# Kernel tuning notes

Measured on AMD Instinct MI355X. Metric: run time of the kernel, lower is better.

The kernel has to match this reference:

```python
import jax, jax.numpy as jnp
import numpy as np

# SNNConfig constants (see init_kwargs)
TAU_MEM = 0.02
TAU_SYN = 0.005
DT = 0.001
THRESHOLD = 1.0
BETA = 10.0  # fast-sigmoid surrogate beta

BATCH, TIME, IN_DIM, HIDDEN = 32, 1024, 512, 512


@jax.custom_vjp
def spike_fn(v):
    """Heaviside spike with fast-sigmoid surrogate gradient."""
    return (v > THRESHOLD).astype(v.dtype)


def _spike_fwd(v):
    return spike_fn(v), v


def _spike_bwd(v, g):
    x = v - THRESHOLD
    surr = 1.0 / jnp.square(1.0 + BETA * jnp.abs(x))
    return (g * surr,)


spike_fn.defvjp(_spike_fwd, _spike_bwd)


def setup_inputs() -> dict:
    key = jax.random.key(0)
    k1, k2 = jax.random.split(key)
    spikes = jax.random.uniform(k1, (BATCH, TIME, IN_DIM), dtype=jnp.float32)
    # xavier_uniform for (IN_DIM, HIDDEN)
    limit = np.sqrt(6.0 / (IN_DIM + HIDDEN))
    W = jax.random.uniform(k2, (IN_DIM, HIDDEN), dtype=jnp.float32,
                           minval=-limit, maxval=limit)
    b = jnp.zeros((HIDDEN,), dtype=jnp.float32)
    return {"spikes": spikes, "W": W, "b": b}


def reference(spikes, W, b):
    # spikes: [B, T, I]; W: [I, H]; b: [H]
    alpha_mem = jnp.exp(jnp.asarray(-DT / TAU_MEM, dtype=spikes.dtype))
    alpha_syn = jnp.exp(jnp.asarray(-DT / TAU_SYN, dtype=spikes.dtype))
    # hoist the per-step GEMM into one big contraction: [B, T, H]
    I_in = jnp.einsum('bti,ih->bth', spikes, W) + b

    B, T, H = I_in.shape
    v0 = jnp.zeros((B, H), dtype=spikes.dtype)
    s0 = jnp.zeros((B, H), dtype=spikes.dtype)

    def lif_step(carry, i_t):
        v_mem, i_syn = carry
        i_syn = alpha_syn * i_syn + i_t
        v_mem = alpha_mem * v_mem + i_syn
        out = spike_fn(v_mem)
        v_mem = v_mem - out * THRESHOLD  # soft reset
        return (v_mem, i_syn), out

    _, out_spikes = jax.lax.scan(lif_step, (v0, s0), I_in.transpose(1, 0, 2))
    return out_spikes.transpose(1, 0, 2)  # [B, T, H]
```

## Files before the change

### kernel.cpp

```cpp
#include <hip/hip_runtime.h>
#include <hip/hip_bf16.h>

constexpr int BATCH  = 32;
constexpr int TIME   = 1024;
constexpr int IN_DIM = 512;
constexpr int HIDDEN = 512;

constexpr int GM = BATCH * TIME;
constexpr int GN = HIDDEN;
constexpr int GK = IN_DIM;

constexpr int BM = 128;
constexpr int BN = 128;
constexpr int BK = 16;
constexpr int LDAs = BM + 4;
constexpr int LDBs = BN + 4;

__global__ __launch_bounds__(256) void sgemm_bias_kernel(
    const float* __restrict__ A,
    const float* __restrict__ B,
    const float* __restrict__ bias,
    float* __restrict__ C)
{
    __shared__ __align__(16) float As[BK * LDAs];
    __shared__ __align__(16) float Bs[BK * LDBs];

    const int tid = threadIdx.x;
    const int bm  = blockIdx.y * BM;
    const int bn  = blockIdx.x * BN;

    const int w    = tid >> 6;
    const int lane = tid & 63;
    const int row0 = (w >> 1) * 64 + (lane >> 3) * 8;
    const int col0 = (w & 1)  * 64 + (lane & 7)  * 8;

    float acc[8][8];
    #pragma unroll
    for (int i = 0; i < 8; ++i)
        #pragma unroll
        for (int j = 0; j < 8; ++j) acc[i][j] = 0.0f;

    for (int k0 = 0; k0 < GK; k0 += BK) {
        float4 va[2], vb[2];
        #pragma unroll
        for (int i = 0; i < 2; ++i) {
            const int q  = tid + i * 256;
            const int ar = q >> 2;
            const int ac = (q & 3) << 2;
            va[i] = *reinterpret_cast<const float4*>(
                A + (size_t)(bm + ar) * GK + k0 + ac);
            const int br = q >> 5;
            const int bc = (q & 31) << 2;
            vb[i] = *reinterpret_cast<const float4*>(
                B + (size_t)(k0 + br) * GN + bn + bc);
        }

        __syncthreads();

        #pragma unroll
        for (int i = 0; i < 2; ++i) {
            const int q  = tid + i * 256;
            const int ar = q >> 2;
            const int ac = (q & 3) << 2;
            As[(ac + 0) * LDAs + ar] = va[i].x;
            As[(ac + 1) * LDAs + ar] = va[i].y;
            As[(ac + 2) * LDAs + ar] = va[i].z;
            As[(ac + 3) * LDAs + ar] = va[i].w;
            const int br = q >> 5;
            const int bc = (q & 31) << 2;
            *reinterpret_cast<float4*>(&Bs[br * LDBs + bc]) = vb[i];
        }

        __syncthreads();

        #pragma unroll
        for (int kk = 0; kk < BK; ++kk) {
            const float4 a0 = *reinterpret_cast<const float4*>(&As[kk * LDAs + row0]);
            const float4 a1 = *reinterpret_cast<const float4*>(&As[kk * LDAs + row0 + 4]);
            const float4 b0 = *reinterpret_cast<const float4*>(&Bs[kk * LDBs + col0]);
            const float4 b1 = *reinterpret_cast<const float4*>(&Bs[kk * LDBs + col0 + 4]);
            const float ar[8] = {a0.x, a0.y, a0.z, a0.w, a1.x, a1.y, a1.z, a1.w};
            const float br[8] = {b0.x, b0.y, b0.z, b0.w, b1.x, b1.y, b1.z, b1.w};
            #pragma unroll
            for (int i = 0; i < 8; ++i)
                #pragma unroll
                for (int j = 0; j < 8; ++j)
                    acc[i][j] = fmaf(ar[i], br[j], acc[i][j]);
        }
    }

    #pragma unroll
    for (int i = 0; i < 8; ++i) {
        const size_t r = (size_t)(bm + row0 + i);
        #pragma unroll
        for (int j = 0; j < 8; j += 4) {
            float4 v;
            v.x = __fadd_rn(acc[i][j + 0], bias[bn + col0 + j + 0]);
            v.y = __fadd_rn(acc[i][j + 1], bias[bn + col0 + j + 1]);
            v.z = __fadd_rn(acc[i][j + 2], bias[bn + col0 + j + 2]);
            v.w = __fadd_rn(acc[i][j + 3], bias[bn + col0 + j + 3]);
            *reinterpret_cast<float4*>(&C[r * GN + bn + col0 + j]) = v;
        }
    }
}

__global__ __launch_bounds__(64) void lif_scan_kernel(
    const float* __restrict__ I,
    float* __restrict__ O)
{
    const int idx = blockIdx.x * 64 + threadIdx.x;
    const int b = idx >> 9;
    const int h = idx & 511;

    const size_t base = (size_t)b * TIME * HIDDEN + h;
    const float* Ip = I + base;
    float*       Op = O + base;

    const float am = 0.95122942450071400910f;
    const float as = 0.81873075307798185867f;

    float v = 0.0f, s = 0.0f;

    #pragma unroll 1
    for (int t = 0; t < TIME; t += 16) {
        float buf[16];
        #pragma unroll
        for (int u = 0; u < 16; ++u)
            buf[u] = Ip[(size_t)(t + u) * HIDDEN];

        float ob[16];
        #pragma unroll
        for (int u = 0; u < 16; ++u) {
            s = __fadd_rn(__fmul_rn(as, s), buf[u]);
            v = __fadd_rn(__fmul_rn(am, v), s);
            const float o = (v > 1.0f) ? 1.0f : 0.0f;
            v = __fsub_rn(v, o);
            ob[u] = o;
        }

        #pragma unroll
        for (int u = 0; u < 16; ++u)
            Op[(size_t)(t + u) * HIDDEN] = ob[u];
    }
}

extern "C" void kernel_launch(void* const* d_in, const int* in_sizes, int n_in,
                              void* d_out, int out_size, void* d_ws, size_t ws_size,
                              hipStream_t stream) {
    const float* spikes = (const float*)d_in[0];
    const float* W      = (const float*)d_in[1];
    const float* bias   = (const float*)d_in[2];
    float* out  = (float*)d_out;
    float* I_in = (float*)d_ws;

    dim3 g1(GN / BN, GM / BM);
    sgemm_bias_kernel<<<g1, 256, 0, stream>>>(spikes, W, bias, I_in);

    lif_scan_kernel<<<BATCH * HIDDEN / 64, 64, 0, stream>>>(I_in, out);
}
```

Before: 340.9 us.

## Double-buffer GEMM shared tiles and prefetch LIF scan input chunks

The SGEMM now keeps two shared-memory buffers and loads the next K tile into registers while computing on the current one, which removes one barrier per iteration. It also swaps the grid mapping so blockIdx.x walks M, and requests 4 blocks per SIMD via launch bounds. The LIF scan kernel prefetches 32-step input chunks into a second register buffer while the current chunk is processed, so more global loads are in flight. Register pressure rises on both kernels, which could cause spilling under the launch bound or lower occupancy.

```diff
diff --git a/kernel.cpp b/kernel.cpp
--- a/kernel.cpp
+++ b/kernel.cpp
@@ -16,23 +16,37 @@
 constexpr int LDAs = BM + 4;
 constexpr int LDBs = BN + 4;
 
-__global__ __launch_bounds__(256) void sgemm_bias_kernel(
+__global__ __launch_bounds__(256, 4) void sgemm_bias_kernel(
     const float* __restrict__ A,
     const float* __restrict__ B,
     const float* __restrict__ bias,
     float* __restrict__ C)
 {
-    __shared__ __align__(16) float As[BK * LDAs];
-    __shared__ __align__(16) float Bs[BK * LDBs];
+    __shared__ __align__(16) float As[2][BK * LDAs];
+    __shared__ __align__(16) float Bs[2][BK * LDBs];
 
     const int tid = threadIdx.x;
-    const int bm  = blockIdx.y * BM;
-    const int bn  = blockIdx.x * BN;
+    const int bm  = blockIdx.x * BM;
+    const int bn  = blockIdx.y * BN;
 
     const int w    = tid >> 6;
     const int lane = tid & 63;
     const int row0 = (w >> 1) * 64 + (lane >> 3) * 8;
     const int col0 = (w & 1)  * 64 + (lane & 7)  * 8;
+
+    const int ar0 = tid >> 2;
+    const int ac  = (tid & 3) << 2;
+    const int br0 = tid >> 5;
+    const int bc  = (tid & 31) << 2;
+
+    float4 va[2], vb[2];
+
+    auto load_tile = [&](int k0) {
+        va[0] = *reinterpret_cast<const float4*>(A + (size_t)(bm + ar0) * GK + k0 + ac);
+        va[1] = *reinterpret_cast<const float4*>(A + (size_t)(bm + ar0 + 64) * GK + k0 + ac);
+        vb[0] = *reinterpret_cast<const float4*>(B + (size_t)(k0 + br0) * GN + bn + bc);
+        vb[1] = *reinterpret_cast<const float4*>(B + (size_t)(k0 + br0 + 8) * GN + bn + bc);
+    };
 
     float acc[8][8];
     #pragma unroll
@@ -40,52 +54,45 @@
         #pragma unroll
         for (int j = 0; j < 8; ++j) acc[i][j] = 0.0f;
 
-    for (int k0 = 0; k0 < GK; k0 += BK) {
-        float4 va[2], vb[2];
-        #pragma unroll
-        for (int i = 0; i < 2; ++i) {
-            const int q  = tid + i * 256;
-            const int ar = q >> 2;
-            const int ac = (q & 3) << 2;
-            va[i] = *reinterpret_cast<const float4*>(
-                A + (size_t)(bm + ar) * GK + k0 + ac);
-            const int br = q >> 5;
-            const int bc = (q & 31) << 2;
-            vb[i] = *reinterpret_cast<const float4*>(
-                B + (size_t)(k0 + br) * GN + bn + bc);
+    load_tile(0);
+
+    constexpr int NTILES = GK / BK;
+    #pragma unroll 1
+    for (int it = 0; it < NTILES; ++it) {
+        const int p = it & 1;
+        float* asp = As[p];
+        float* bsp = Bs[p];
+
+        {
+            asp[(ac + 0) * LDAs + ar0] = va[0].x;
+            asp[(ac + 1) * LDAs + ar0] = va[0].y;
+            asp[(ac + 2) * LDAs + ar0] = va[0].z;
+            asp[(ac + 3) * LDAs + ar0] = va[0].w;
+            asp[(ac + 0) * LDAs + ar0 + 64] = va[1].x;
+            asp[(ac + 1) * LDAs + ar0 + 64] = va[1].y;
+            asp[(ac + 2) * LDAs + ar0 + 64] = va[1].z;
+            asp[(ac + 3) * LDAs + ar0 + 64] = va[1].w;
+            *reinterpret_cast<float4*>(&bsp[br0 * LDBs + bc]) = vb[0];
+            *reinterpret_cast<float4*>(&bsp[(br0 + 8) * LDBs + bc]) = vb[1];
         }
 
         __syncthreads();
 
-        #pragma unroll
-        for (int i = 0; i < 2; ++i) {
-            const int q  = tid + i * 256;
-            const int ar = q >> 2;
-            const int ac = (q & 3) << 2;
-            As[(ac + 0) * LDAs + ar] = va[i].x;
-            As[(ac + 1) * LDAs + ar] = va[i].y;
-            As[(ac + 2) * LDAs + ar] = va[i].z;
-            As[(ac + 3) * LDAs + ar] = va[i].w;
-            const int br = q >> 5;
-            const int bc = (q & 31) << 2;
-            *reinterpret_cast<float4*>(&Bs[br * LDBs + bc]) = vb[i];
-        }
-
-        __syncthreads();
+        if (it + 1 < NTILES) load_tile((it + 1) * BK);
 
         #pragma unroll
         for (int kk = 0; kk < BK; ++kk) {
-            const float4 a0 = *reinterpret_cast<const float4*>(&As[kk * LDAs + row0]);
-            const float4 a1 = *reinterpret_cast<const float4*>(&As[kk * LDAs + row0 + 4]);
-            const float4 b0 = *reinterpret_cast<const float4*>(&Bs[kk * LDBs + col0]);
-            const float4 b1 = *reinterpret_cast<const float4*>(&Bs[kk * LDBs + col0 + 4]);
-            const float ar[8] = {a0.x, a0.y, a0.z, a0.w, a1.x, a1.y, a1.z, a1.w};
-            const float br[8] = {b0.x, b0.y, b0.z, b0.w, b1.x, b1.y, b1.z, b1.w};
+            const float4 a0 = *reinterpret_cast<const float4*>(&asp[kk * LDAs + row0]);
+            const float4 a1 = *reinterpret_cast<const float4*>(&asp[kk * LDAs + row0 + 4]);
+            const float4 b0 = *reinterpret_cast<const float4*>(&bsp[kk * LDBs + col0]);
+            const float4 b1 = *reinterpret_cast<const float4*>(&bsp[kk * LDBs + col0 + 4]);
+            const float arr[8] = {a0.x, a0.y, a0.z, a0.w, a1.x, a1.y, a1.z, a1.w};
+            const float brr[8] = {b0.x, b0.y, b0.z, b0.w, b1.x, b1.y, b1.z, b1.w};
             #pragma unroll
             for (int i = 0; i < 8; ++i)
                 #pragma unroll
                 for (int j = 0; j < 8; ++j)
-                    acc[i][j] = fmaf(ar[i], br[j], acc[i][j]);
+                    acc[i][j] = fmaf(arr[i], brr[j], acc[i][j]);
         }
     }
 
@@ -104,6 +111,9 @@
     }
 }
 
+constexpr int CH = 32;
+constexpr int NCH = TIME / CH;
+
 __global__ __launch_bounds__(64) void lif_scan_kernel(
     const float* __restrict__ I,
     float* __restrict__ O)
@@ -120,27 +130,53 @@
     const float as = 0.81873075307798185867f;
 
     float v = 0.0f, s = 0.0f;
+    float bufA[CH], bufB[CH];
+
+    #pragma unroll
+    for (int u = 0; u < CH; ++u)
+        bufA[u] = Ip[(size_t)u * HIDDEN];
 
     #pragma unroll 1
-    for (int t = 0; t < TIME; t += 16) {
-        float buf[16];
+    for (int c = 0; c < NCH; c += 2) {
         #pragma unroll
-        for (int u = 0; u < 16; ++u)
-            buf[u] = Ip[(size_t)(t + u) * HIDDEN];
+        for (int u = 0; u < CH; ++u)
+            bufB[u] = Ip[(size_t)((c + 1) * CH + u) * HIDDEN];
 
-        float ob[16];
-        #pragma unroll
-        for (int u = 0; u < 16; ++u) {
-            s = __fadd_rn(__fmul_rn(as, s), buf[u]);
-            v = __fadd_rn(__fmul_rn(am, v), s);
-            const float o = (v > 1.0f) ? 1.0f : 0.0f;
-            v = __fsub_rn(v, o);
-            ob[u] = o;
+        {
+            float ob[CH];
+            #pragma unroll
+            for (int u = 0; u < CH; ++u) {
+                s = __fadd_rn(__fmul_rn(as, s), bufA[u]);
+                v = __fadd_rn(__fmul_rn(am, v), s);
+                const float o = (v > 1.0f) ? 1.0f : 0.0f;
+                v = __fsub_rn(v, o);
+                ob[u] = o;
+            }
+            #pragma unroll
+            for (int u = 0; u < CH; ++u)
+                Op[(size_t)(c * CH + u) * HIDDEN] = ob[u];
         }
 
-        #pragma unroll
-        for (int u = 0; u < 16; ++u)
-            Op[(size_t)(t + u) * HIDDEN] = ob[u];
+        if (c + 2 < NCH) {
+            #pragma unroll
+            for (int u = 0; u < CH; ++u)
+                bufA[u] = Ip[(size_t)((c + 2) * CH + u) * HIDDEN];
+        }
+
+        {
+            float ob[CH];
+            #pragma unroll
+            for (int u = 0; u < CH; ++u) {
+                s = __fadd_rn(__fmul_rn(as, s), bufB[u]);
+                v = __fadd_rn(__fmul_rn(am, v), s);
+                const float o = (v > 1.0f) ? 1.0f : 0.0f;
+                v = __fsub_rn(v, o);
+                ob[u] = o;
+            }
+            #pragma unroll
+            for (int u = 0; u < CH; ++u)
+                Op[(size_t)((c + 1) * CH + u) * HIDDEN] = ob[u];
+        }
     }
 }
 
@@ -153,7 +189,7 @@
     float* out  = (float*)d_out;
     float* I_in = (float*)d_ws;
 
-    dim3 g1(GN / BN, GM / BM);
+    dim3 g1(GM / BM, GN / BN);
     sgemm_bias_kernel<<<g1, 256, 0, stream>>>(spikes, W, bias, I_in);
 
     lif_scan_kernel<<<BATCH * HIDDEN / 64, 64, 0, stream>>>(I_in, out);
```

New measurement: 1.054 ms. 209% more time.

## Fuse GEMM and LIF scan into one warp-specialized kernel with LDS ring

Applied to the files above, without the earlier changes.

Replaces the separate SGEMM and scan kernels with a single kernel. Each block owns one batch and 64 hidden units. Four waves compute 256-timestep chunks of the input current into a double-buffered LDS ring, while a fifth wave runs the LIF recurrence on the previous chunk in lockstep through shared barriers. This removes the 64 MB intermediate write and read-back and the second launch. In exchange it uses about 149 KB of LDS per block, so only one block fits per CU, with only four compute waves and little latency hiding. It also uses a narrower 64-column tile, which makes A be re-read more often.

```diff
diff --git a/kernel.cpp b/kernel.cpp
--- a/kernel.cpp
+++ b/kernel.cpp
@@ -6,141 +6,150 @@
 constexpr int IN_DIM = 512;
 constexpr int HIDDEN = 512;
 
-constexpr int GM = BATCH * TIME;
-constexpr int GN = HIDDEN;
-constexpr int GK = IN_DIM;
+constexpr int TC   = 256;
+constexpr int NC   = TIME / TC;
+constexpr int BK   = 16;
+constexpr int NKT  = IN_DIM / BK;
+constexpr int LDA2 = TC + 4;
+constexpr int LDB2 = 64 + 4;
 
-constexpr int BM = 128;
-constexpr int BN = 128;
-constexpr int BK = 16;
-constexpr int LDAs = BM + 4;
-constexpr int LDBs = BN + 4;
+__global__ __launch_bounds__(320) void fused_lif_kernel(
+    const float* __restrict__ A,
+    const float* __restrict__ Bw,
+    const float* __restrict__ bias,
+    float* __restrict__ O)
+{
+    __shared__ __align__(16) float As[BK * LDA2];
+    __shared__ __align__(16) float Bs[BK * LDB2];
+    __shared__ __align__(16) float ring[2][TC * 64];
 
-__global__ __launch_bounds__(256) void sgemm_bias_kernel(
-    const float* __restrict__ A,
-    const float* __restrict__ B,
-    const float* __restrict__ bias,
-    float* __restrict__ C)
-{
-    __shared__ __align__(16) float As[BK * LDAs];
-    __shared__ __align__(16) float Bs[BK * LDBs];
+    const int blk  = blockIdx.x;
+    const int b    = blk >> 3;
+    const int h0   = (blk & 7) * 64;
+    const int wave = threadIdx.x >> 6;
+    const int lane = threadIdx.x & 63;
 
-    const int tid = threadIdx.x;
-    const int bm  = blockIdx.y * BM;
-    const int bn  = blockIdx.x * BN;
+    const float* Ab = A + (size_t)b * TIME * IN_DIM;
 
-    const int w    = tid >> 6;
-    const int lane = tid & 63;
-    const int row0 = (w >> 1) * 64 + (lane >> 3) * 8;
-    const int col0 = (w & 1)  * 64 + (lane & 7)  * 8;
+    if (wave < 4) {
+        const int tid = threadIdx.x;
+        const int ar = tid >> 2;
+        const int ac = (tid & 3) << 2;
+        const int br = tid >> 4;
+        const int bc = (tid & 15) << 2;
+        const int row0 = wave * 64 + (lane >> 3) * 8;
+        const int col0 = (lane & 7) * 8;
 
-    float acc[8][8];
-    #pragma unroll
-    for (int i = 0; i < 8; ++i)
-        #pragma unroll
-        for (int j = 0; j < 8; ++j) acc[i][j] = 0.0f;
+        float4 va[4], vb;
+        auto load_tile = [&](int c, int kt) {
+            const float* Ap = Ab + (size_t)(c * TC) * IN_DIM + kt * BK;
+            #pragma unroll
+            for (int q = 0; q < 4; ++q)
+                va[q] = *reinterpret_cast<const float4*>(
+                    Ap + (size_t)(ar + 64 * q) * IN_DIM + ac);
+            vb = *reinterpret_cast<const float4*>(
+                Bw + (size_t)(kt * BK + br) * HIDDEN + h0 + bc);
+        };
+        auto store_tile = [&]() {
+            #pragma unroll
+            for (int q = 0; q < 4; ++q) {
+                As[(ac + 0) * LDA2 + ar + 64 * q] = va[q].x;
+                As[(ac + 1) * LDA2 + ar + 64 * q] = va[q].y;
+                As[(ac + 2) * LDA2 + ar + 64 * q] = va[q].z;
+                As[(ac + 3) * LDA2 + ar + 64 * q] = va[q].w;
+            }
+            *reinterpret_cast<float4*>(&Bs[br * LDB2 + bc]) = vb;
+        };
 
-    for (int k0 = 0; k0 < GK; k0 += BK) {
-        float4 va[2], vb[2];
-        #pragma unroll
-        for (int i = 0; i < 2; ++i) {
-            const int q  = tid + i * 256;
-            const int ar = q >> 2;
-            const int ac = (q & 3) << 2;
-            va[i] = *reinterpret_cast<const float4*>(
-                A + (size_t)(bm + ar) * GK + k0 + ac);
-            const int br = q >> 5;
-            const int bc = (q & 31) << 2;
-            vb[i] = *reinterpret_cast<const float4*>(
-                B + (size_t)(k0 + br) * GN + bn + bc);
-        }
-
-        __syncthreads();
-
-        #pragma unroll
-        for (int i = 0; i < 2; ++i) {
-            const int q  = tid + i * 256;
-            const int ar = q >> 2;
-            const int ac = (q & 3) << 2;
-            As[(ac + 0) * LDAs + ar] = va[i].x;
-            As[(ac + 1) * LDAs + ar] = va[i].y;
-            As[(ac + 2) * LDAs + ar] = va[i].z;
-            As[(ac + 3) * LDAs + ar] = va[i].w;
-            const int br = q >> 5;
-            const int bc = (q & 31) << 2;
-            *reinterpret_cast<float4*>(&Bs[br * LDBs + bc]) = vb[i];
-        }
-
-        __syncthreads();
-
-        #pragma unroll
-        for (int kk = 0; kk < BK; ++kk) {
-            const float4 a0 = *reinterpret_cast<const float4*>(&As[kk * LDAs + row0]);
-            const float4 a1 = *reinterpret_cast<const float4*>(&As[kk * LDAs + row0 + 4]);
-            const float4 b0 = *reinterpret_cast<const float4*>(&Bs[kk * LDBs + col0]);
-            const float4 b1 = *reinterpret_cast<const float4*>(&Bs[kk * LDBs + col0 + 4]);
-            const float ar[8] = {a0.x, a0.y, a0.z, a0.w, a1.x, a1.y, a1.z, a1.w};
-            const float br[8] = {b0.x, b0.y, b0.z, b0.w, b1.x, b1.y, b1.z, b1.w};
+        #pragma unroll 1
+        for (int c = 0; c < NC; ++c) {
+            float acc[8][8];
             #pragma unroll
             for (int i = 0; i < 8; ++i)
                 #pragma unroll
-                for (int j = 0; j < 8; ++j)
-                    acc[i][j] = fmaf(ar[i], br[j], acc[i][j]);
+                for (int j = 0; j < 8; ++j) acc[i][j] = 0.0f;
+
+            load_tile(c, 0);
+
+            #pragma unroll 1
+            for (int kt = 0; kt < NKT; ++kt) {
+                __syncthreads();
+                store_tile();
+                if (kt + 1 < NKT) load_tile(c, kt + 1);
+                __syncthreads();
+
+                #pragma unroll
+                for (int kk = 0; kk < BK; ++kk) {
+                    const float4 a0 = *reinterpret_cast<const float4*>(&As[kk * LDA2 + row0]);
+                    const float4 a1 = *reinterpret_cast<const float4*>(&As[kk * LDA2 + row0 + 4]);
+                    const float4 b0 = *reinterpret_cast<const float4*>(&Bs[kk * LDB2 + col0]);
+                    const float4 b1 = *reinterpret_cast<const float4*>(&Bs[kk * LDB2 + col0 + 4]);
+                    const float arr[8] = {a0.x, a0.y, a0.z, a0.w, a1.x, a1.y, a1.z, a1.w};
+                    const float brr[8] = {b0.x, b0.y, b0.z, b0.w, b1.x, b1.y, b1.z, b1.w};
+                    #pragma unroll
+                    for (int i = 0; i < 8; ++i)
+                        #pragma unroll
+                        for (int j = 0; j < 8; ++j)
+                            acc[i][j] = fmaf(arr[i], brr[j], acc[i][j]);
+                }
+            }
+
+            float* rp = ring[c & 1];
+            #pragma unroll
+            for (int i = 0; i < 8; ++i) {
+                #pragma unroll
+                for (int j = 0; j < 8; j += 4) {
+                    float4 v;
+                    v.x = __fadd_rn(acc[i][j + 0], bias[h0 + col0 + j + 0]);
+                    v.y = __fadd_rn(acc[i][j + 1], bias[h0 + col0 + j + 1]);
+                    v.z = __fadd_rn(acc[i][j + 2], bias[h0 + col0 + j + 2]);
+                    v.w = __fadd_rn(acc[i][j + 3], bias[h0 + col0 + j + 3]);
+                    *reinterpret_cast<float4*>(&rp[(row0 + i) * 64 + col0 + j]) = v;
+                }
+            }
+            __syncthreads();
         }
-    }
+    } else {
+        const float am = 0.95122942450071400910f;
+        const float as = 0.81873075307798185867f;
+        float v = 0.0f, s = 0.0f;
+        float* o0 = O + (size_t)b * TIME * HIDDEN + h0 + lane;
 
-    #pragma unroll
-    for (int i = 0; i < 8; ++i) {
-        const size_t r = (size_t)(bm + row0 + i);
-        #pragma unroll
-        for (int j = 0; j < 8; j += 4) {
-            float4 v;
-            v.x = __fadd_rn(acc[i][j + 0], bias[bn + col0 + j + 0]);
-            v.y = __fadd_rn(acc[i][j + 1], bias[bn + col0 + j + 1]);
-            v.z = __fadd_rn(acc[i][j + 2], bias[bn + col0 + j + 2]);
-            v.w = __fadd_rn(acc[i][j + 3], bias[bn + col0 + j + 3]);
-            *reinterpret_cast<float4*>(&C[r * GN + bn + col0 + j]) = v;
+        auto slice = [&](const float* rp, int tbase, int tglob) {
+            float xb[8];
+            #pragma unroll
+            for (int u = 0; u < 8; ++u)
+                xb[u] = rp[(tbase + u) * 64 + lane];
+            float ob[8];
+            #pragma unroll
+            for (int u = 0; u < 8; ++u) {
+                s = __fadd_rn(__fmul_rn(as, s), xb[u]);
+                v = __fadd_rn(__fmul_rn(am, v), s);
+                const float o = (v > 1.0f) ? 1.0f : 0.0f;
+                v = __fsub_rn(v, o);
+                ob[u] = o;
+            }
+            #pragma unroll
+            for (int u = 0; u < 8; ++u)
+                o0[(size_t)(tglob + u) * HIDDEN] = ob[u];
+        };
+
+        #pragma unroll 1
+        for (int c = 0; c < NC; ++c) {
+            const float* rp = ring[(c + 1) & 1];
+            #pragma unroll 1
+            for (int kt = 0; kt < NKT; ++kt) {
+                __syncthreads();
+                __syncthreads();
+                if (c > 0)
+                    slice(rp, kt * 8, (c - 1) * TC + kt * 8);
+            }
+            __syncthreads();
         }
-    }
-}
-
-__global__ __launch_bounds__(64) void lif_scan_kernel(
-    const float* __restrict__ I,
-    float* __restrict__ O)
-{
-    const int idx = blockIdx.x * 64 + threadIdx.x;
-    const int b = idx >> 9;
-    const int h = idx & 511;
-
-    const size_t base = (size_t)b * TIME * HIDDEN + h;
-    const float* Ip = I + base;
-    float*       Op = O + base;
-
-    const float am = 0.95122942450071400910f;
-    const float as = 0.81873075307798185867f;
-
-    float v = 0.0f, s = 0.0f;
-
-    #pragma unroll 1
-    for (int t = 0; t < TIME; t += 16) {
-        float buf[16];
-        #pragma unroll
-        for (int u = 0; u < 16; ++u)
-            buf[u] = Ip[(size_t)(t + u) * HIDDEN];
-
-        float ob[16];
-        #pragma unroll
-        for (int u = 0; u < 16; ++u) {
-            s = __fadd_rn(__fmul_rn(as, s), buf[u]);
-            v = __fadd_rn(__fmul_rn(am, v), s);
-            const float o = (v > 1.0f) ? 1.0f : 0.0f;
-            v = __fsub_rn(v, o);
-            ob[u] = o;
-        }
-
-        #pragma unroll
-        for (int u = 0; u < 16; ++u)
-            Op[(size_t)(t + u) * HIDDEN] = ob[u];
+        const float* rp = ring[(NC - 1) & 1];
+        #pragma unroll 1
+        for (int kt = 0; kt < NKT; ++kt)
+            slice(rp, kt * 8, (NC - 1) * TC + kt * 8);
     }
 }
 
@@ -150,11 +159,7 @@
     const float* spikes = (const float*)d_in[0];
     const float* W      = (const float*)d_in[1];
     const float* bias   = (const float*)d_in[2];
-    float* out  = (float*)d_out;
-    float* I_in = (float*)d_ws;
+    float* out = (float*)d_out;
 
-    dim3 g1(GN / BN, GM / BM);
-    sgemm_bias_kernel<<<g1, 256, 0, stream>>>(spikes, W, bias, I_in);
-
-    lif_scan_kernel<<<BATCH * HIDDEN / 64, 64, 0, stream>>>(I_in, out);
+    fused_lif_kernel<<<256, 320, 0, stream>>>(spikes, W, bias, out);
 }
```

After: 372.2 us. +9.2%, slower.
